# Kernel tuning notes

Measured on AMD Instinct MI355X. Metric: run time of the kernel, lower is better.

## Reference

```python
import jax, jax.numpy as jnp
import numpy as np

NUM = 32768
DIM = 2048
NUM_CLASSES = 512
EPS = 1e-6  # torch F.pairwise_distance adds eps to the difference


def setup_inputs() -> dict:
    key = jax.random.key(0)
    k1, k2 = jax.random.split(key)
    output = jax.random.normal(k1, (NUM, DIM), dtype=jnp.float32)
    label_id = jax.random.randint(k2, (NUM,), 0, NUM_CLASSES, dtype=jnp.int64)
    return {"output": output, "label_id": label_id}


def reference(output, label_id):
    # Per-label mean of features (segment mean), replacing the O(n^2) python loop.
    ones = jnp.ones((output.shape[0],), dtype=output.dtype)
    counts = jax.ops.segment_sum(ones, label_id, num_segments=NUM_CLASSES)  # [C]
    sums = jax.ops.segment_sum(output, label_id, num_segments=NUM_CLASSES)  # [C, D]
    means = sums / jnp.maximum(counts, 1.0)[:, None]
    # output2[i] = mean of class of sample i
    diff = output - means[label_id] + EPS  # [N, D]
    # pairwise_distance(...)**2 == sum of squared (diff + eps); mean over samples
    sq_dist = jnp.sum(diff * diff, axis=1)  # [N]
    return jnp.mean(sq_dist)
```

## Files before the change

### kernel.cpp

```cpp
#include <hip/hip_runtime.h>

constexpr int NSAMP = 32768;
constexpr int DIM   = 2048;
constexpr int NCLS  = 512;
constexpr double EPS = 1e-6;
constexpr int NSLICE = 8;
constexpr int NPART  = NSLICE * NCLS;
constexpr int CAP    = 160;


__global__ void __launch_bounds__(256) k_fill(const int* __restrict__ label,
                                              int* __restrict__ cursors,
                                              int* __restrict__ idx) {
    const int i = blockIdx.x * 256 + threadIdx.x;
    if (i < NSAMP) {
        const int c = label[i];
        const int p = atomicAdd(&cursors[c], 1);
        if (p < CAP) idx[c * CAP + p] = i;
    }
}

__global__ void __launch_bounds__(64) k_main(const float* __restrict__ x,
                                             const int* __restrict__ cursors,
                                             const int* __restrict__ idx,
                                             double* __restrict__ partQ,
                                             double* __restrict__ partT) {
    const int c   = blockIdx.y;
    const int s   = blockIdx.x;
    const int cnt = min(cursors[c], CAP);
    __shared__ int idx_lds[CAP];
    for (int r = threadIdx.x; r < cnt; r += 64)
        idx_lds[r] = idx[c * CAP + r];
    __syncthreads();

    const float* xp = x + s * 256 + threadIdx.x * 4;

    float SxA = 0.f, SyA = 0.f, SzA = 0.f, SwA = 0.f;
    float SxB = 0.f, SyB = 0.f, SzB = 0.f, SwB = 0.f;
    float QA = 0.f, QB = 0.f;

    int r = 0;
    for (; r + 8 <= cnt; r += 8) {
        int id[8];
        #pragma unroll
        for (int j = 0; j < 8; ++j) id[j] = idx_lds[r + j];
        float4 v[8];
        #pragma unroll
        for (int j = 0; j < 8; ++j)
            v[j] = *reinterpret_cast<const float4*>(xp + (size_t)id[j] * DIM);
        #pragma unroll
        for (int j = 0; j < 8; j += 2) {
            SxA += v[j].x; SyA += v[j].y; SzA += v[j].z; SwA += v[j].w;
            QA += v[j].x*v[j].x + v[j].y*v[j].y + v[j].z*v[j].z + v[j].w*v[j].w;
            SxB += v[j+1].x; SyB += v[j+1].y; SzB += v[j+1].z; SwB += v[j+1].w;
            QB += v[j+1].x*v[j+1].x + v[j+1].y*v[j+1].y + v[j+1].z*v[j+1].z + v[j+1].w*v[j+1].w;
        }
    }
    for (; r < cnt; ++r) {
        const int i0 = idx_lds[r];
        const float4 a = *reinterpret_cast<const float4*>(xp + (size_t)i0 * DIM);
        SxA += a.x; SyA += a.y; SzA += a.z; SwA += a.w;
        QA += a.x*a.x + a.y*a.y + a.z*a.z + a.w*a.w;
    }

    const float Sx = SxA + SxB, Sy = SyA + SyB, Sz = SzA + SzB, Sw = SwA + SwB;
    double s2 = (double)Sx*(double)Sx + (double)Sy*(double)Sy
              + (double)Sz*(double)Sz + (double)Sw*(double)Sw;
    double q  = (double)(QA + QB);

    #pragma unroll
    for (int off = 32; off > 0; off >>= 1) {
        q  += __shfl_down(q,  off, 64);
        s2 += __shfl_down(s2, off, 64);
    }
    if (threadIdx.x == 0) {
        const int slot = c * NSLICE + s;
        partQ[slot] = q;
        partT[slot] = (cnt > 0) ? (s2 / (double)cnt) : 0.0;
    }
}

__global__ void __launch_bounds__(256) k_final(const double* __restrict__ partQ,
                                               const double* __restrict__ partT,
                                               float* __restrict__ out) {
    double q = 0.0, t3 = 0.0;
    for (int i = threadIdx.x; i < NPART; i += 256) {
        q  += partQ[i];
        t3 += partT[i];
    }
    __shared__ double sq[256], st[256];
    sq[threadIdx.x] = q;
    st[threadIdx.x] = t3;
    __syncthreads();
    for (int o = 128; o > 0; o >>= 1) {
        if (threadIdx.x < o) {
            sq[threadIdx.x] += sq[threadIdx.x + o];
            st[threadIdx.x] += st[threadIdx.x + o];
        }
        __syncthreads();
    }
    if (threadIdx.x == 0) {
        out[0] = (float)((sq[0] - st[0]) / (double)NSAMP + (double)DIM * EPS * EPS);
    }
}

extern "C" void kernel_launch(void* const* d_in, const int* in_sizes, int n_in,
                              void* d_out, int out_size, void* d_ws, size_t ws_size,
                              hipStream_t stream) {
    const float* x     = (const float*)d_in[0];
    const int*   label = (const int*)d_in[1];
    float*       out   = (float*)d_out;

    char* ws = (char*)d_ws;
    int*    cursors = (int*)(ws + 0);
    int*    idx     = (int*)(ws + 8192);
    double* partQ   = (double*)(ws + 344064);
    double* partT   = (double*)(ws + 376832);

    hipMemsetAsync(cursors, 0, NCLS * sizeof(int), stream);
    hipLaunchKernelGGL(k_fill, dim3(NSAMP / 256), dim3(256), 0, stream,
                       label, cursors, idx);
    hipLaunchKernelGGL(k_main, dim3(NSLICE, NCLS), dim3(64), 0, stream,
                       x, cursors, idx, partQ, partT);
    hipLaunchKernelGGL(k_final, dim3(1), dim3(256), 0, stream, partQ, partT, out);
}
```

Baseline: 68.46 us.

## Halve column slices per class and scramble block-to-class mapping

Each 64-thread block now covers 512 columns (two float4 loads per row) instead of 256, so there are 4 slices per class instead of 8 and twice the loads in flight per thread. The grid is flattened to 1D and each block's class is picked with a multiplicative hash, spreading concurrently running blocks across classes and rows of memory. Each index list is read by half as many blocks, while register use goes up and the grid shrinks to 2048 blocks. The bijection (331 odd, 57*s mod 512) keeps the class coverage correct.

```diff
diff --git a/kernel.cpp b/kernel.cpp
--- a/kernel.cpp
+++ b/kernel.cpp
@@ -4,7 +4,7 @@
 constexpr int DIM   = 2048;
 constexpr int NCLS  = 512;
 constexpr double EPS = 1e-6;
-constexpr int NSLICE = 8;
+constexpr int NSLICE = 4;
 constexpr int NPART  = NSLICE * NCLS;
 constexpr int CAP    = 160;
 
@@ -25,15 +25,18 @@
                                              const int* __restrict__ idx,
                                              double* __restrict__ partQ,
                                              double* __restrict__ partT) {
-    const int c   = blockIdx.y;
-    const int s   = blockIdx.x;
+    const int b  = blockIdx.x;
+    const int q0 = b >> 2;
+    const int s  = b & 3;
+    const int c  = (q0 * 331 + s * 57) & 511;
     const int cnt = min(cursors[c], CAP);
     __shared__ int idx_lds[CAP];
     for (int r = threadIdx.x; r < cnt; r += 64)
         idx_lds[r] = idx[c * CAP + r];
     __syncthreads();
 
-    const float* xp = x + s * 256 + threadIdx.x * 4;
+    const float* xpA = x + s * 512 + threadIdx.x * 4;
+    const float* xpB = xpA + 256;
 
     float SxA = 0.f, SyA = 0.f, SzA = 0.f, SwA = 0.f;
     float SxB = 0.f, SyB = 0.f, SzB = 0.f, SwB = 0.f;
@@ -41,31 +44,35 @@
 
     int r = 0;
     for (; r + 8 <= cnt; r += 8) {
-        int id[8];
+        float4 va[8], vb[8];
         #pragma unroll
-        for (int j = 0; j < 8; ++j) id[j] = idx_lds[r + j];
-        float4 v[8];
+        for (int j = 0; j < 8; ++j) {
+            const size_t ro = (size_t)idx_lds[r + j] * DIM;
+            va[j] = *reinterpret_cast<const float4*>(xpA + ro);
+            vb[j] = *reinterpret_cast<const float4*>(xpB + ro);
+        }
         #pragma unroll
-        for (int j = 0; j < 8; ++j)
-            v[j] = *reinterpret_cast<const float4*>(xp + (size_t)id[j] * DIM);
-        #pragma unroll
-        for (int j = 0; j < 8; j += 2) {
-            SxA += v[j].x; SyA += v[j].y; SzA += v[j].z; SwA += v[j].w;
-            QA += v[j].x*v[j].x + v[j].y*v[j].y + v[j].z*v[j].z + v[j].w*v[j].w;
-            SxB += v[j+1].x; SyB += v[j+1].y; SzB += v[j+1].z; SwB += v[j+1].w;
-            QB += v[j+1].x*v[j+1].x + v[j+1].y*v[j+1].y + v[j+1].z*v[j+1].z + v[j+1].w*v[j+1].w;
+        for (int j = 0; j < 8; ++j) {
+            SxA += va[j].x; SyA += va[j].y; SzA += va[j].z; SwA += va[j].w;
+            QA += va[j].x*va[j].x + va[j].y*va[j].y + va[j].z*va[j].z + va[j].w*va[j].w;
+            SxB += vb[j].x; SyB += vb[j].y; SzB += vb[j].z; SwB += vb[j].w;
+            QB += vb[j].x*vb[j].x + vb[j].y*vb[j].y + vb[j].z*vb[j].z + vb[j].w*vb[j].w;
         }
     }
     for (; r < cnt; ++r) {
-        const int i0 = idx_lds[r];
-        const float4 a = *reinterpret_cast<const float4*>(xp + (size_t)i0 * DIM);
+        const size_t ro = (size_t)idx_lds[r] * DIM;
+        const float4 a = *reinterpret_cast<const float4*>(xpA + ro);
+        const float4 d = *reinterpret_cast<const float4*>(xpB + ro);
         SxA += a.x; SyA += a.y; SzA += a.z; SwA += a.w;
         QA += a.x*a.x + a.y*a.y + a.z*a.z + a.w*a.w;
+        SxB += d.x; SyB += d.y; SzB += d.z; SwB += d.w;
+        QB += d.x*d.x + d.y*d.y + d.z*d.z + d.w*d.w;
     }
 
-    const float Sx = SxA + SxB, Sy = SyA + SyB, Sz = SzA + SzB, Sw = SwA + SwB;
-    double s2 = (double)Sx*(double)Sx + (double)Sy*(double)Sy
-              + (double)Sz*(double)Sz + (double)Sw*(double)Sw;
+    double s2 = (double)SxA*(double)SxA + (double)SyA*(double)SyA
+              + (double)SzA*(double)SzA + (double)SwA*(double)SwA
+              + (double)SxB*(double)SxB + (double)SyB*(double)SyB
+              + (double)SzB*(double)SzB + (double)SwB*(double)SwB;
     double q  = (double)(QA + QB);
 
     #pragma unroll
@@ -115,12 +122,12 @@
     int*    cursors = (int*)(ws + 0);
     int*    idx     = (int*)(ws + 8192);
     double* partQ   = (double*)(ws + 344064);
-    double* partT   = (double*)(ws + 376832);
+    double* partT   = (double*)(ws + 360448);
 
     hipMemsetAsync(cursors, 0, NCLS * sizeof(int), stream);
     hipLaunchKernelGGL(k_fill, dim3(NSAMP / 256), dim3(256), 0, stream,
                        label, cursors, idx);
-    hipLaunchKernelGGL(k_main, dim3(NSLICE, NCLS), dim3(64), 0, stream,
+    hipLaunchKernelGGL(k_main, dim3(NSLICE * NCLS), dim3(64), 0, stream,
                        x, cursors, idx, partQ, partT);
     hipLaunchKernelGGL(k_final, dim3(1), dim3(256), 0, stream, partQ, partT, out);
 }
```

New measurement: 66.04 us. 3.5% less time.
